# Performance work log

Measured on AMD Instinct MI355X. Metric: run time of the kernel, lower is better.

## Reference

```python
import jax, jax.numpy as jnp
import numpy as np
from jax.ops import segment_sum, segment_max

N, E, FIN, H, C, L, G, ED = 50000, 400000, 256, 4, 64, 3, 25, 2
D = H * C  # 256 = dim*heads


def setup_inputs() -> dict:
    key = jax.random.key(0)
    k = jax.random.split(key, 16)
    s = 0.05
    f = jnp.float32
    return {
        "x": jax.random.normal(k[0], (N, FIN), f),
        "edge_attr": jax.random.uniform(k[1], (E, ED), dtype=f),
        "edge_index": jax.random.randint(k[2], (2, E), 0, N),
        "batch": jnp.sort(jax.random.randint(k[3], (N,), 0, G)),
        "W_pre": jax.random.normal(k[4], (FIN, D), f) * s,
        "b_pre": jnp.zeros((D,), f),
        "W_src": jax.random.normal(k[5], (L, D, D), f) * s,
        "W_dst": jax.random.normal(k[6], (L, D, D), f) * s,
        "W_edge": jax.random.normal(k[7], (L, ED, D), f) * s,
        "att_src": jax.random.normal(k[8], (L, H, C), f) * s,
        "att_dst": jax.random.normal(k[9], (L, H, C), f) * s,
        "att_edge": jax.random.normal(k[10], (L, H, C), f) * s,
        "bias_conv": jnp.zeros((L, D), f),
        "ln_gamma": jnp.ones((L, D), f),
        "ln_beta": jnp.zeros((L, D), f),
        "prelu_a": jnp.full((L, D), 0.25, f),
        "W_post1": jax.random.normal(k[11], (D * (L + 1), D), f) * s,
        "b_post1": jnp.zeros((D,), f),
        "W_post2": jax.random.normal(k[12], (D, D), f) * s,
        "b_post2": jnp.zeros((D,), f),
        "W_risk": jax.random.normal(k[13], (D, 1), f) * s,
        "b_risk": jnp.zeros((1,), f),
    }


def _segment_mean(v, seg, num):
    tot = segment_sum(v, seg, num_segments=num)
    cnt = segment_sum(jnp.ones((v.shape[0], 1), v.dtype), seg, num_segments=num)
    return tot / jnp.maximum(cnt, 1.0)


def _layer_norm(h, g, b, eps=1e-5):
    mu = jnp.mean(h, -1, keepdims=True)
    var = jnp.var(h, -1, keepdims=True)
    return (h - mu) * jax.lax.rsqrt(var + eps) * g + b


def _gat_forward(x, edge_attr, edge_index, batch, params):
    (W_pre, b_pre, W_src, W_dst, W_edge, att_src, att_dst, att_edge,
     bias_conv, ln_gamma, ln_beta, prelu_a,
     W_post1, b_post1, W_post2, b_post2, W_risk, b_risk) = params
    row, col = edge_index[0], edge_index[1]  # src -> dst
    # preprocess: project raw node features to D = dim*heads
    h = x @ W_pre + b_pre  # [N, D]
    concat = [_segment_mean(h, batch, G)]  # x0_glob
    for l in range(L):  # fixed small layer count
        xs = (h @ W_src[l]).reshape(N, H, C)
        xd = (h @ W_dst[l]).reshape(N, H, C)
        ea = (edge_attr @ W_edge[l]).reshape(E, H, C)
        # edge-wise attention logits [E, H]
        a = ((xs * att_src[l]).sum(-1)[row]
             + (xd * att_dst[l]).sum(-1)[col]
             + (ea * att_edge[l]).sum(-1))
        a = jax.nn.leaky_relu(a, 0.2)
        # segment softmax over destination nodes
        m = segment_max(a, col, num_segments=N)
        w = jnp.exp(a - m[col])
        z = segment_sum(w, col, num_segments=N)
        alpha = w / (z[col] + 1e-16)  # [E, H]
        # weighted message passing: gather src feats, scatter-add to dst
        out = segment_sum(xs[row] * alpha[:, :, None], col, num_segments=N)
        out = out.reshape(N, D) + bias_conv[l]
        # per-graph LayerNorm loop == single row-wise LayerNorm
        out = _layer_norm(out, ln_gamma[l], ln_beta[l])
        # channel-wise PReLU
        out = jnp.where(out > 0, out, prelu_a[l] * out)
        concat.append(_segment_mean(out, batch, G))
        h = out + h  # residual_connection == 'Y'
    xc = jnp.concatenate(concat, axis=1)  # [G, D*(L+1)]
    p = jax.nn.relu(xc @ W_post1 + b_post1)
    p = jax.nn.relu(p @ W_post2 + b_post2)
    return p @ W_risk + b_risk  # [G, 1] risk


def reference(x, edge_attr, edge_index, batch, W_pre, b_pre, W_src, W_dst,
              W_edge, att_src, att_dst, att_edge, bias_conv, ln_gamma,
              ln_beta, prelu_a, W_post1, b_post1, W_post2, b_post2,
              W_risk, b_risk):
    params = (W_pre, b_pre, W_src, W_dst, W_edge, att_src, att_dst, att_edge,
              bias_conv, ln_gamma, ln_beta, prelu_a,
              W_post1, b_post1, W_post2, b_post2, W_risk, b_risk)
    return _gat_forward(x, edge_attr, edge_index, batch, params)
```

## Files before the change

kernel.cpp:

```cpp
#include <hip/hip_runtime.h>
#include <math.h>

#define NN 50000
#define NPAD 50048
#define EE 400000
#define DD 256
#define HH 4
#define CC 64
#define LL 3
#define GG 25

typedef _Float16 half4_t __attribute__((ext_vector_type(4)));
typedef _Float16 half8_t __attribute__((ext_vector_type(8)));
typedef float f32x4_t __attribute__((ext_vector_type(4)));

__global__ __launch_bounds__(256) void gemm_mfma(
    const _Float16* __restrict__ Ahi, const _Float16* __restrict__ Alo,
    const _Float16* __restrict__ Bhi, const _Float16* __restrict__ Blo,
    const float* __restrict__ bias, float* __restrict__ C, int N)
{
  __shared__ _Float16 lds[4][128][32];
  const int t = threadIdx.x;
  const int wave = t >> 6, lane = t & 63;
  const int m0 = blockIdx.x * 128, bn0 = blockIdx.y * 128;
  const int wm = wave >> 1, wn = wave & 1;

  f32x4_t acc[4][4];
#pragma unroll
  for (int i = 0; i < 4; i++)
#pragma unroll
    for (int j = 0; j < 4; j++) acc[i][j] = (f32x4_t){0.f, 0.f, 0.f, 0.f};

  const int l15 = lane & 15, kg = lane >> 4;
  int aoff[4], boff[4];
#pragma unroll
  for (int tr = 0; tr < 4; tr++) {
    int r = wm * 64 + tr * 16 + l15;
    aoff[tr] = r * 64 + ((kg ^ ((r >> 1) & 3)) * 16);
    int n = wn * 64 + tr * 16 + l15;
    boff[tr] = n * 64 + ((kg ^ ((n >> 1) & 3)) * 16);
  }

  const _Float16* gsrc[4];
  gsrc[0] = Ahi + (size_t)m0 * 256;
  gsrc[1] = Alo + (size_t)m0 * 256;
  gsrc[2] = Bhi + (size_t)bn0 * 256;
  gsrc[3] = Blo + (size_t)bn0 * 256;

  const char* lbase = (const char*)&lds[0][0][0];

  for (int k0 = 0; k0 < DD; k0 += 32) {
    __syncthreads();
#pragma unroll
    for (int b = 0; b < 4; b++) {
#pragma unroll
      for (int c = 0; c < 2; c++) {
        int rowbase = (wave << 5) + (c << 4);
        const _Float16* g = gsrc[b] + (size_t)(rowbase + (lane >> 2)) * 256
                            + k0 + (lane & 3) * 8;
        char* l = (char*)lbase + b * 8192 + rowbase * 64;
        __builtin_amdgcn_global_load_lds(
            (const __attribute__((address_space(1))) void*)g,
            (__attribute__((address_space(3))) void*)l, 16, 0, 0);
      }
    }
    __syncthreads();

    half8_t ah[4], al[4], bh[4], bl[4];
#pragma unroll
    for (int i = 0; i < 4; i++) {
      ah[i] = *(const half8_t*)(lbase + 0 * 8192 + aoff[i]);
      al[i] = *(const half8_t*)(lbase + 1 * 8192 + aoff[i]);
      bh[i] = *(const half8_t*)(lbase + 2 * 8192 + boff[i]);
      bl[i] = *(const half8_t*)(lbase + 3 * 8192 + boff[i]);
    }
#pragma unroll
    for (int i = 0; i < 4; i++)
#pragma unroll
      for (int j = 0; j < 4; j++) {
        acc[i][j] = __builtin_amdgcn_mfma_f32_16x16x32_f16(ah[i], bh[j], acc[i][j], 0, 0, 0);
        acc[i][j] = __builtin_amdgcn_mfma_f32_16x16x32_f16(ah[i], bl[j], acc[i][j], 0, 0, 0);
        acc[i][j] = __builtin_amdgcn_mfma_f32_16x16x32_f16(al[i], bh[j], acc[i][j], 0, 0, 0);
      }
  }

#pragma unroll
  for (int i = 0; i < 4; i++) {
    int rb = m0 + wm * 64 + i * 16 + (lane >> 4) * 4;
#pragma unroll
    for (int j = 0; j < 4; j++) {
      int col = bn0 + wn * 64 + j * 16 + l15;
      float bv = bias ? bias[col] : 0.f;
#pragma unroll
      for (int q = 0; q < 4; q++) {
        int r = rb + q;
        if (r < N) C[(size_t)r * DD + col] = acc[i][j][q] + bv;
      }
    }
  }
}

__global__ __launch_bounds__(256) void split_f16(
    const float* __restrict__ src, _Float16* __restrict__ hi,
    _Float16* __restrict__ lo, int N)
{
  int f = blockIdx.x * 256 + threadIdx.x;
  if (f >= N * 64) return;
  int m = f >> 6, q = f & 63;
  float4 v = *(const float4*)(src + (size_t)f * 4);
  int gp = (q >> 1) ^ ((m >> 1) & 3);
  int off = m * 256 + gp * 8 + (q & 1) * 4;
  half4_t h4, l4;
  h4[0] = (_Float16)v.x; l4[0] = (_Float16)(v.x - (float)h4[0]);
  h4[1] = (_Float16)v.y; l4[1] = (_Float16)(v.y - (float)h4[1]);
  h4[2] = (_Float16)v.z; l4[2] = (_Float16)(v.z - (float)h4[2]);
  h4[3] = (_Float16)v.w; l4[3] = (_Float16)(v.w - (float)h4[3]);
  *(half4_t*)(hi + off) = h4;
  *(half4_t*)(lo + off) = l4;
}

__global__ void prep_w(const float* __restrict__ W, _Float16* __restrict__ bhi,
                       _Float16* __restrict__ blo)
{
  int n = blockIdx.x, k = threadIdx.x;
  float v = W[(size_t)k * DD + n];
  _Float16 h = (_Float16)v, l = (_Float16)(v - (float)h);
  int kp = (((k >> 3) ^ ((n >> 1) & 3)) << 3) | (k & 7);
  bhi[(size_t)n * DD + kp] = h;
  blo[(size_t)n * DD + kp] = l;
}

__global__ void prep_att(const float* __restrict__ Ws, const float* __restrict__ Wd,
                         const float* __restrict__ We, const float* __restrict__ as_,
                         const float* __restrict__ ad_, const float* __restrict__ ae_,
                         float* __restrict__ wmat, float* __restrict__ wea)
{
  int l = blockIdx.x;
  int t = threadIdx.x;
  for (int idx = t; idx < DD * 8; idx += 256) {
    int k = idx >> 3, hd = idx & 7;
    const float* W; const float* att; int hh;
    if (hd < 4) { W = Ws; att = as_; hh = hd; }
    else        { W = Wd; att = ad_; hh = hd - 4; }
    const float* wrow = W + (size_t)l * DD * DD + (size_t)k * DD + hh * CC;
    const float* arow = att + l * DD + hh * CC;
    float s = 0.f;
#pragma unroll 4
    for (int c = 0; c < CC; c++) s = fmaf(wrow[c], arow[c], s);
    wmat[(size_t)l * DD * 8 + idx] = s;
  }
  if (t < 8) {
    int d = t >> 2, hh = t & 3;
    const float* wrow = We + (size_t)l * 2 * DD + (size_t)d * DD + hh * CC;
    const float* arow = ae_ + l * DD + hh * CC;
    float s = 0.f;
#pragma unroll 4
    for (int c = 0; c < CC; c++) s = fmaf(wrow[c], arow[c], s);
    wea[l * 8 + d * 4 + hh] = s;
  }
}

__global__ void graph_bounds(const int* __restrict__ batch, int* __restrict__ goff,
                             int N, int G)
{
  int g = threadIdx.x;
  if (g > G) return;
  int lo = 0, hi = N;
  while (lo < hi) { int mid = (lo + hi) >> 1; if (batch[mid] < g) lo = mid + 1; else hi = mid; }
  goff[g] = lo;
}

__global__ void hist_col(const int* __restrict__ ei, int* __restrict__ deg, int E)
{
  int e = blockIdx.x * 256 + threadIdx.x;
  if (e < E) atomicAdd(&deg[ei[E + e]], 1);
}

__global__ void scan1(const int* __restrict__ deg, int* __restrict__ incl,
                      int* __restrict__ bsum, int N)
{
  __shared__ int sm[256];
  int b = blockIdx.x, t = threadIdx.x;
  int i = b * 256 + t;
  int v = (i < N) ? deg[i] : 0;
  sm[t] = v;
  __syncthreads();
  for (int off = 1; off < 256; off <<= 1) {
    int add = (t >= off) ? sm[t - off] : 0;
    __syncthreads();
    sm[t] += add;
    __syncthreads();
  }
  if (i < N) incl[i] = sm[t];
  if (t == 255) bsum[b] = sm[255];
}

__global__ void scan2(int* __restrict__ bsum, int nb)
{
  if (threadIdx.x == 0 && blockIdx.x == 0) {
    int run = 0;
    for (int i = 0; i < nb; i++) { int v = bsum[i]; bsum[i] = run; run += v; }
  }
}

__global__ void scan3(const int* __restrict__ deg, const int* __restrict__ incl,
                      const int* __restrict__ bsum, int* __restrict__ rowptr,
                      int* __restrict__ cur, int N, int E)
{
  int i = blockIdx.x * 256 + threadIdx.x;
  if (i < N) {
    int ex = incl[i] - deg[i] + bsum[blockIdx.x];
    rowptr[i] = ex;
    cur[i] = ex;
  }
  if (i == 0) rowptr[N] = E;
}

__global__ void scatter_edges(const int* __restrict__ ei, const float* __restrict__ eattr,
                              int* __restrict__ cur, int* __restrict__ srow,
                              float2* __restrict__ sea, int E)
{
  int e = blockIdx.x * 256 + threadIdx.x;
  if (e < E) {
    int c = ei[E + e];
    int p = atomicAdd(&cur[c], 1);
    srow[p] = ei[e];
    sea[p] = ((const float2*)eattr)[e];
  }
}

__global__ __launch_bounds__(256) void att_proj(
    const float* __restrict__ h, const float* __restrict__ wmatL,
    float* __restrict__ asrc, float* __restrict__ adst, int N)
{
  __shared__ float Hs[32][260];
  __shared__ float Wm[DD * 8];
  int t = threadIdx.x;
  for (int i = t; i < DD * 8; i += 256) Wm[i] = wmatL[i];
  int n0 = blockIdx.x * 32;
  for (int i = t; i < 32 * 64; i += 256) {
    int n = i >> 6, c4 = i & 63;
    float4 v = {0.f, 0.f, 0.f, 0.f};
    if (n0 + n < N) v = *(const float4*)(h + (size_t)(n0 + n) * DD + c4 * 4);
    Hs[n][c4 * 4 + 0] = v.x; Hs[n][c4 * 4 + 1] = v.y;
    Hs[n][c4 * 4 + 2] = v.z; Hs[n][c4 * 4 + 3] = v.w;
  }
  __syncthreads();
  int n = t >> 3, hd = t & 7;
  float s0 = 0, s1 = 0, s2 = 0, s3 = 0;
  for (int k = 0; k < DD; k += 4) {
    s0 = fmaf(Hs[n][k + 0], Wm[(k + 0) * 8 + hd], s0);
    s1 = fmaf(Hs[n][k + 1], Wm[(k + 1) * 8 + hd], s1);
    s2 = fmaf(Hs[n][k + 2], Wm[(k + 2) * 8 + hd], s2);
    s3 = fmaf(Hs[n][k + 3], Wm[(k + 3) * 8 + hd], s3);
  }
  float s = (s0 + s1) + (s2 + s3);
  int gn = n0 + n;
  if (gn < N) {
    if (hd < 4) asrc[gn * 4 + hd] = s;
    else        adst[gn * 4 + (hd - 4)] = s;
  }
}

__global__ __launch_bounds__(256) void dst_fused(
    const float* __restrict__ xs, const float* __restrict__ asrc,
    const float* __restrict__ adst, const int* __restrict__ rowptr,
    const int* __restrict__ srow, const float2* __restrict__ sea,
    const float* __restrict__ weaL, const float* __restrict__ biasL,
    const float* __restrict__ gL, const float* __restrict__ bL,
    const float* __restrict__ pL, float* __restrict__ h,
    _Float16* __restrict__ hhi, _Float16* __restrict__ hlo, int N)
{
  int wid = blockIdx.x * 4 + (threadIdx.x >> 6);
  int lane = threadIdx.x & 63;
  if (wid >= N) return;
  const int head = lane >> 4;
  const int start = rowptr[wid];
  const int end = rowptr[wid + 1];
  const float ad = adst[wid * 4 + head];
  const float w0 = weaL[head];
  const float w1 = weaL[4 + head];
  float ax = 0.f, ay = 0.f, az = 0.f, aw = 0.f;
  float z = 0.f;
  int p = start;
  for (; p + 2 <= end; p += 2) {
    int r0 = srow[p], r1 = srow[p + 1];
    float2 e0 = sea[p], e1 = sea[p + 1];
    float s0 = asrc[r0 * 4 + head], s1 = asrc[r1 * 4 + head];
    float4 x0 = *(const float4*)(xs + (size_t)r0 * DD + lane * 4);
    float4 x1 = *(const float4*)(xs + (size_t)r1 * DD + lane * 4);
    float a0 = s0 + ad + e0.x * w0 + e0.y * w1;
    a0 = a0 > 0.f ? a0 : 0.2f * a0;
    float wt0 = expf(a0);
    float a1 = s1 + ad + e1.x * w0 + e1.y * w1;
    a1 = a1 > 0.f ? a1 : 0.2f * a1;
    float wt1 = expf(a1);
    z += wt0 + wt1;
    ax = fmaf(wt0, x0.x, ax); ay = fmaf(wt0, x0.y, ay);
    az = fmaf(wt0, x0.z, az); aw = fmaf(wt0, x0.w, aw);
    ax = fmaf(wt1, x1.x, ax); ay = fmaf(wt1, x1.y, ay);
    az = fmaf(wt1, x1.z, az); aw = fmaf(wt1, x1.w, aw);
  }
  if (p < end) {
    int r = srow[p];
    float2 ea = sea[p];
    float a = asrc[r * 4 + head] + ad + ea.x * w0 + ea.y * w1;
    a = a > 0.f ? a : 0.2f * a;
    float wt = expf(a);
    z += wt;
    float4 xv = *(const float4*)(xs + (size_t)r * DD + lane * 4);
    ax = fmaf(wt, xv.x, ax); ay = fmaf(wt, xv.y, ay);
    az = fmaf(wt, xv.z, az); aw = fmaf(wt, xv.w, aw);
  }
  float inv = 1.f / (z + 1e-16f);
  float4 bi = *(const float4*)(biasL + lane * 4);
  float o0 = ax * inv + bi.x;
  float o1 = ay * inv + bi.y;
  float o2 = az * inv + bi.z;
  float o3 = aw * inv + bi.w;
  float s = (o0 + o1) + (o2 + o3);
  float q = (o0 * o0 + o1 * o1) + (o2 * o2 + o3 * o3);
#pragma unroll
  for (int off = 32; off; off >>= 1) {
    s += __shfl_xor(s, off, 64);
    q += __shfl_xor(q, off, 64);
  }
  float mu = s * (1.f / 256.f);
  float var = q * (1.f / 256.f) - mu * mu;
  float rs = rsqrtf(var + 1e-5f);
  float4 gg = *(const float4*)(gL + lane * 4);
  float4 bb = *(const float4*)(bL + lane * 4);
  float4 pp = *(const float4*)(pL + lane * 4);
  o0 = (o0 - mu) * rs * gg.x + bb.x;  o0 = o0 > 0.f ? o0 : pp.x * o0;
  o1 = (o1 - mu) * rs * gg.y + bb.y;  o1 = o1 > 0.f ? o1 : pp.y * o1;
  o2 = (o2 - mu) * rs * gg.z + bb.z;  o2 = o2 > 0.f ? o2 : pp.z * o2;
  o3 = (o3 - mu) * rs * gg.w + bb.w;  o3 = o3 > 0.f ? o3 : pp.w * o3;
  float4 hv = *(const float4*)(h + (size_t)wid * DD + lane * 4);
  float4 ov;
  ov.x = o0 + hv.x; ov.y = o1 + hv.y; ov.z = o2 + hv.z; ov.w = o3 + hv.w;
  *(float4*)(h + (size_t)wid * DD + lane * 4) = ov;
  if (hhi) {
    int gp = (lane >> 1) ^ ((wid >> 1) & 3);
    int off2 = wid * DD + gp * 8 + (lane & 1) * 4;
    half4_t h4, l4;
    h4[0] = (_Float16)ov.x; l4[0] = (_Float16)(ov.x - (float)h4[0]);
    h4[1] = (_Float16)ov.y; l4[1] = (_Float16)(ov.y - (float)h4[1]);
    h4[2] = (_Float16)ov.z; l4[2] = (_Float16)(ov.z - (float)h4[2]);
    h4[3] = (_Float16)ov.w; l4[3] = (_Float16)(ov.w - (float)h4[3]);
    *(half4_t*)(hhi + off2) = h4;
    *(half4_t*)(hlo + off2) = l4;
  }
}

__global__ void mean_accum(const float* __restrict__ x, const int* __restrict__ goff,
                           float* __restrict__ msum)
{
  int g = blockIdx.x, sp = blockIdx.y, t = threadIdx.x;
  int lo = goff[g], hi = goff[g + 1];
  int cnt = hi - lo;
  if (cnt <= 0) return;
  int per = (cnt + gridDim.y - 1) / gridDim.y;
  int st = lo + sp * per;
  int en = min(hi, st + per);
  if (st >= en) return;
  float acc = 0.f;
  for (int n = st; n < en; ++n) acc += x[(size_t)n * DD + t];
  atomicAdd(&msum[g * DD + t], acc);
}

__global__ void mean_fin(const float* __restrict__ msum, const int* __restrict__ goff,
                         float* __restrict__ dst)
{
  int g = blockIdx.x, t = threadIdx.x;
  int cnt = goff[g + 1] - goff[g];
  dst[g * DD + t] = msum[g * DD + t] / fmaxf((float)cnt, 1.f);
}

__global__ __launch_bounds__(256) void head_mlp(
    const float* __restrict__ hmean, const float* __restrict__ W1,
    const float* __restrict__ b1, const float* __restrict__ W2,
    const float* __restrict__ b2, const float* __restrict__ Wr,
    const float* __restrict__ br, float* __restrict__ out)
{
  __shared__ float xc[4 * DD];
  __shared__ float p1[DD];
  __shared__ float red[256];
  int g = blockIdx.x, t = threadIdx.x;
  float m0 = hmean[0 * GG * DD + g * DD + t];
  float m1 = hmean[1 * GG * DD + g * DD + t];
  float m2 = hmean[2 * GG * DD + g * DD + t];
  float m3 = hmean[3 * GG * DD + g * DD + t];
  xc[t] = m0;
  xc[DD + t] = m1 - m0;
  xc[2 * DD + t] = m2 - m1;
  xc[3 * DD + t] = m3 - m2;
  __syncthreads();
  float acc = b1[t];
  for (int k = 0; k < 4 * DD; k++) acc = fmaf(xc[k], W1[(size_t)k * DD + t], acc);
  p1[t] = fmaxf(acc, 0.f);
  __syncthreads();
  float acc2 = b2[t];
  for (int k = 0; k < DD; k++) acc2 = fmaf(p1[k], W2[(size_t)k * DD + t], acc2);
  float v = fmaxf(acc2, 0.f) * Wr[t];
  red[t] = v;
  __syncthreads();
  for (int sdown = 128; sdown; sdown >>= 1) {
    if (t < sdown) red[t] += red[t + sdown];
    __syncthreads();
  }
  if (t == 0) out[g] = red[0] + br[0];
}

extern "C" void kernel_launch(void* const* d_in, const int* in_sizes, int n_in,
                              void* d_out, int out_size, void* d_ws, size_t ws_size,
                              hipStream_t stream)
{
  const float* x        = (const float*)d_in[0];
  const float* eattr    = (const float*)d_in[1];
  const int*   eidx     = (const int*)d_in[2];
  const int*   batch    = (const int*)d_in[3];
  const float* W_pre    = (const float*)d_in[4];
  const float* b_pre    = (const float*)d_in[5];
  const float* W_src    = (const float*)d_in[6];
  const float* W_dst    = (const float*)d_in[7];
  const float* W_edge   = (const float*)d_in[8];
  const float* att_src  = (const float*)d_in[9];
  const float* att_dst  = (const float*)d_in[10];
  const float* att_edge = (const float*)d_in[11];
  const float* bias_conv= (const float*)d_in[12];
  const float* ln_g     = (const float*)d_in[13];
  const float* ln_b     = (const float*)d_in[14];
  const float* prelu    = (const float*)d_in[15];
  const float* W1       = (const float*)d_in[16];
  const float* b1       = (const float*)d_in[17];
  const float* W2       = (const float*)d_in[18];
  const float* b2       = (const float*)d_in[19];
  const float* Wr       = (const float*)d_in[20];
  const float* br       = (const float*)d_in[21];
  float* out = (float*)d_out;

  char* w = (char*)d_ws;
  size_t off = 0;
  auto alloc = [&](size_t bytes) -> char* {
    char* p = w + off;
    off += (bytes + 255) & ~(size_t)255;
    return p;
  };
  float*     h     = (float*)alloc((size_t)NN * DD * 4);
  char*      xsreg = alloc((size_t)NPAD * DD * 4);
  float*     xs    = (float*)xsreg;
  _Float16*  x_hi  = (_Float16*)xsreg;
  _Float16*  x_lo  = (_Float16*)(xsreg + (size_t)NPAD * DD * 2);
  _Float16*  h_hi  = (_Float16*)alloc((size_t)NPAD * DD * 2);
  _Float16*  h_lo  = (_Float16*)alloc((size_t)NPAD * DD * 2);
  _Float16*  bt_hi = (_Float16*)alloc((size_t)4 * DD * DD * 2);
  _Float16*  bt_lo = (_Float16*)alloc((size_t)4 * DD * DD * 2);
  float*  asrc  = (float*)alloc((size_t)NN * HH * 4);
  float*  adst  = (float*)alloc((size_t)NN * HH * 4);
  float*  wmat  = (float*)alloc((size_t)LL * DD * 8 * 4);
  float*  wea   = (float*)alloc((size_t)LL * 8 * 4);
  float*  hmean = (float*)alloc((size_t)(LL + 1) * GG * DD * 4);
  float*  msum  = (float*)alloc((size_t)GG * DD * 4);
  float2* sea   = (float2*)alloc((size_t)EE * 8);
  int*    goff  = (int*)alloc((GG + 1) * 4);
  int*    deg   = (int*)alloc((size_t)NN * 4);
  int*    rowptr= (int*)alloc((size_t)(NN + 1) * 4);
  int*    cur   = (int*)alloc((size_t)NN * 4);
  int*    incl  = (int*)alloc((size_t)NN * 4);
  int*    bsum  = (int*)alloc(256 * 4);
  int*    srow  = (int*)alloc((size_t)EE * 4);
  if (off > ws_size) return;

  prep_att<<<dim3(LL), dim3(256), 0, stream>>>(W_src, W_dst, W_edge, att_src,
                                               att_dst, att_edge, wmat, wea);
  prep_w<<<dim3(DD), dim3(DD), 0, stream>>>(W_pre, bt_hi, bt_lo);
  for (int l = 0; l < LL; l++)
    prep_w<<<dim3(DD), dim3(DD), 0, stream>>>(W_src + (size_t)l * DD * DD,
                                              bt_hi + (size_t)(l + 1) * DD * DD,
                                              bt_lo + (size_t)(l + 1) * DD * DD);
  graph_bounds<<<dim3(1), dim3(32), 0, stream>>>(batch, goff, NN, GG);
  hipMemsetAsync(deg, 0, (size_t)NN * 4, stream);
  hist_col<<<dim3((EE + 255) / 256), dim3(256), 0, stream>>>(eidx, deg, EE);
  int nb = (NN + 255) / 256;
  scan1<<<dim3(nb), dim3(256), 0, stream>>>(deg, incl, bsum, NN);
  scan2<<<dim3(1), dim3(1), 0, stream>>>(bsum, nb);
  scan3<<<dim3(nb), dim3(256), 0, stream>>>(deg, incl, bsum, rowptr, cur, NN, EE);
  scatter_edges<<<dim3((EE + 255) / 256), dim3(256), 0, stream>>>(eidx, eattr, cur,
                                                                  srow, sea, EE);

  split_f16<<<dim3((NN * 64 + 255) / 256), dim3(256), 0, stream>>>(x, x_hi, x_lo, NN);
  dim3 gg((NN + 127) / 128, 2);
  gemm_mfma<<<gg, dim3(256), 0, stream>>>(x_hi, x_lo, bt_hi, bt_lo, b_pre, h, NN);
  split_f16<<<dim3((NN * 64 + 255) / 256), dim3(256), 0, stream>>>(h, h_hi, h_lo, NN);
  hipMemsetAsync(msum, 0, (size_t)GG * DD * 4, stream);
  mean_accum<<<dim3(GG, 16), dim3(DD), 0, stream>>>(h, goff, msum);
  mean_fin<<<dim3(GG), dim3(DD), 0, stream>>>(msum, goff, hmean);

  for (int l = 0; l < LL; l++) {
    gemm_mfma<<<gg, dim3(256), 0, stream>>>(h_hi, h_lo,
                                            bt_hi + (size_t)(l + 1) * DD * DD,
                                            bt_lo + (size_t)(l + 1) * DD * DD,
                                            (const float*)nullptr, xs, NN);
    att_proj<<<dim3((NN + 31) / 32), dim3(256), 0, stream>>>(h, wmat + (size_t)l * DD * 8,
                                                             asrc, adst, NN);
    bool ws = (l < LL - 1);
    dst_fused<<<dim3((NN + 3) / 4), dim3(256), 0, stream>>>(
        xs, asrc, adst, rowptr, srow, sea, wea + l * 8, bias_conv + l * DD,
        ln_g + l * DD, ln_b + l * DD, prelu + l * DD, h,
        ws ? h_hi : (_Float16*)nullptr, ws ? h_lo : (_Float16*)nullptr, NN);
    hipMemsetAsync(msum, 0, (size_t)GG * DD * 4, stream);
    mean_accum<<<dim3(GG, 16), dim3(DD), 0, stream>>>(h, goff, msum);
    mean_fin<<<dim3(GG), dim3(DD), 0, stream>>>(msum, goff,
                                                hmean + (size_t)(l + 1) * GG * DD);
  }

  head_mlp<<<dim3(GG), dim3(256), 0, stream>>>(hmean, W1, b1, W2, b2, Wr, br, out);
}
```

Measured before the change: 982.4 us.

## Double-buffer GEMM LDS, unroll edge loop, fuse next-layer attention projection

```diff
diff --git a/kernel.cpp b/kernel.cpp
--- a/kernel.cpp
+++ b/kernel.cpp
@@ -19,7 +19,7 @@
     const _Float16* __restrict__ Bhi, const _Float16* __restrict__ Blo,
     const float* __restrict__ bias, float* __restrict__ C, int N)
 {
-  __shared__ _Float16 lds[4][128][32];
+  __shared__ _Float16 lds[2][4][128][32];
   const int t = threadIdx.x;
   const int wave = t >> 6, lane = t & 63;
   const int m0 = blockIdx.x * 128, bn0 = blockIdx.y * 128;
@@ -47,32 +47,39 @@
   gsrc[2] = Bhi + (size_t)bn0 * 256;
   gsrc[3] = Blo + (size_t)bn0 * 256;
 
-  const char* lbase = (const char*)&lds[0][0][0];
-
-  for (int k0 = 0; k0 < DD; k0 += 32) {
-    __syncthreads();
+  char* lbase = (char*)&lds[0][0][0][0];
+  const int rowbase0 = (wave << 5);
+
+  auto stage = [&](int buf, int k0) {
 #pragma unroll
     for (int b = 0; b < 4; b++) {
 #pragma unroll
       for (int c = 0; c < 2; c++) {
-        int rowbase = (wave << 5) + (c << 4);
+        int rowbase = rowbase0 + (c << 4);
         const _Float16* g = gsrc[b] + (size_t)(rowbase + (lane >> 2)) * 256
                             + k0 + (lane & 3) * 8;
-        char* l = (char*)lbase + b * 8192 + rowbase * 64;
+        char* l = lbase + (size_t)(buf * 4 + b) * 8192 + rowbase * 64;
         __builtin_amdgcn_global_load_lds(
             (const __attribute__((address_space(1))) void*)g,
             (__attribute__((address_space(3))) void*)l, 16, 0, 0);
       }
     }
-    __syncthreads();
-
+  };
+
+  stage(0, 0);
+  __syncthreads();
+  int cur = 0;
+  for (int k0 = 0; k0 < DD; k0 += 32) {
+    if (k0 + 32 < DD) stage(cur ^ 1, k0 + 32);
+
+    const char* lb = lbase + (size_t)cur * 4 * 8192;
     half8_t ah[4], al[4], bh[4], bl[4];
 #pragma unroll
     for (int i = 0; i < 4; i++) {
-      ah[i] = *(const half8_t*)(lbase + 0 * 8192 + aoff[i]);
-      al[i] = *(const half8_t*)(lbase + 1 * 8192 + aoff[i]);
-      bh[i] = *(const half8_t*)(lbase + 2 * 8192 + boff[i]);
-      bl[i] = *(const half8_t*)(lbase + 3 * 8192 + boff[i]);
+      ah[i] = *(const half8_t*)(lb + 0 * 8192 + aoff[i]);
+      al[i] = *(const half8_t*)(lb + 1 * 8192 + aoff[i]);
+      bh[i] = *(const half8_t*)(lb + 2 * 8192 + boff[i]);
+      bl[i] = *(const half8_t*)(lb + 3 * 8192 + boff[i]);
     }
 #pragma unroll
     for (int i = 0; i < 4; i++)
@@ -82,6 +89,8 @@
         acc[i][j] = __builtin_amdgcn_mfma_f32_16x16x32_f16(ah[i], bl[j], acc[i][j], 0, 0, 0);
         acc[i][j] = __builtin_amdgcn_mfma_f32_16x16x32_f16(al[i], bh[j], acc[i][j], 0, 0, 0);
       }
+    __syncthreads();
+    cur ^= 1;
   }
 
 #pragma unroll
@@ -269,7 +278,9 @@
     const float* __restrict__ weaL, const float* __restrict__ biasL,
     const float* __restrict__ gL, const float* __restrict__ bL,
     const float* __restrict__ pL, float* __restrict__ h,
-    _Float16* __restrict__ hhi, _Float16* __restrict__ hlo, int N)
+    _Float16* __restrict__ hhi, _Float16* __restrict__ hlo,
+    const float* __restrict__ wnext, float* __restrict__ asrcN,
+    float* __restrict__ adstN, int N)
 {
   int wid = blockIdx.x * 4 + (threadIdx.x >> 6);
   int lane = threadIdx.x & 63;
@@ -283,30 +294,51 @@
   float ax = 0.f, ay = 0.f, az = 0.f, aw = 0.f;
   float z = 0.f;
   int p = start;
+  for (; p + 4 <= end; p += 4) {
+    int r0 = srow[p], r1 = srow[p + 1], r2 = srow[p + 2], r3 = srow[p + 3];
+    float2 e0 = sea[p], e1 = sea[p + 1], e2 = sea[p + 2], e3 = sea[p + 3];
+    float s0 = asrc[r0 * 4 + head], s1 = asrc[r1 * 4 + head];
+    float s2 = asrc[r2 * 4 + head], s3 = asrc[r3 * 4 + head];
+    float4 x0 = *(const float4*)(xs + (size_t)r0 * DD + lane * 4);
+    float4 x1 = *(const float4*)(xs + (size_t)r1 * DD + lane * 4);
+    float4 x2 = *(const float4*)(xs + (size_t)r2 * DD + lane * 4);
+    float4 x3 = *(const float4*)(xs + (size_t)r3 * DD + lane * 4);
+    float a0 = s0 + ad + e0.x * w0 + e0.y * w1; a0 = a0 > 0.f ? a0 : 0.2f * a0;
+    float a1 = s1 + ad + e1.x * w0 + e1.y * w1; a1 = a1 > 0.f ? a1 : 0.2f * a1;
+    float a2 = s2 + ad + e2.x * w0 + e2.y * w1; a2 = a2 > 0.f ? a2 : 0.2f * a2;
+    float a3 = s3 + ad + e3.x * w0 + e3.y * w1; a3 = a3 > 0.f ? a3 : 0.2f * a3;
+    float t0 = __expf(a0), t1 = __expf(a1), t2 = __expf(a2), t3 = __expf(a3);
+    z += (t0 + t1) + (t2 + t3);
+    ax = fmaf(t0, x0.x, ax); ay = fmaf(t0, x0.y, ay);
+    az = fmaf(t0, x0.z, az); aw = fmaf(t0, x0.w, aw);
+    ax = fmaf(t1, x1.x, ax); ay = fmaf(t1, x1.y, ay);
+    az = fmaf(t1, x1.z, az); aw = fmaf(t1, x1.w, aw);
+    ax = fmaf(t2, x2.x, ax); ay = fmaf(t2, x2.y, ay);
+    az = fmaf(t2, x2.z, az); aw = fmaf(t2, x2.w, aw);
+    ax = fmaf(t3, x3.x, ax); ay = fmaf(t3, x3.y, ay);
+    az = fmaf(t3, x3.z, az); aw = fmaf(t3, x3.w, aw);
+  }
   for (; p + 2 <= end; p += 2) {
     int r0 = srow[p], r1 = srow[p + 1];
     float2 e0 = sea[p], e1 = sea[p + 1];
     float s0 = asrc[r0 * 4 + head], s1 = asrc[r1 * 4 + head];
     float4 x0 = *(const float4*)(xs + (size_t)r0 * DD + lane * 4);
     float4 x1 = *(const float4*)(xs + (size_t)r1 * DD + lane * 4);
-    float a0 = s0 + ad + e0.x * w0 + e0.y * w1;
-    a0 = a0 > 0.f ? a0 : 0.2f * a0;
-    float wt0 = expf(a0);
-    float a1 = s1 + ad + e1.x * w0 + e1.y * w1;
-    a1 = a1 > 0.f ? a1 : 0.2f * a1;
-    float wt1 = expf(a1);
-    z += wt0 + wt1;
-    ax = fmaf(wt0, x0.x, ax); ay = fmaf(wt0, x0.y, ay);
-    az = fmaf(wt0, x0.z, az); aw = fmaf(wt0, x0.w, aw);
-    ax = fmaf(wt1, x1.x, ax); ay = fmaf(wt1, x1.y, ay);
-    az = fmaf(wt1, x1.z, az); aw = fmaf(wt1, x1.w, aw);
+    float a0 = s0 + ad + e0.x * w0 + e0.y * w1; a0 = a0 > 0.f ? a0 : 0.2f * a0;
+    float a1 = s1 + ad + e1.x * w0 + e1.y * w1; a1 = a1 > 0.f ? a1 : 0.2f * a1;
+    float t0 = __expf(a0), t1 = __expf(a1);
+    z += t0 + t1;
+    ax = fmaf(t0, x0.x, ax); ay = fmaf(t0, x0.y, ay);
+    az = fmaf(t0, x0.z, az); aw = fmaf(t0, x0.w, aw);
+    ax = fmaf(t1, x1.x, ax); ay = fmaf(t1, x1.y, ay);
+    az = fmaf(t1, x1.z, az); aw = fmaf(t1, x1.w, aw);
   }
   if (p < end) {
     int r = srow[p];
     float2 ea = sea[p];
     float a = asrc[r * 4 + head] + ad + ea.x * w0 + ea.y * w1;
     a = a > 0.f ? a : 0.2f * a;
-    float wt = expf(a);
+    float wt = __expf(a);
     z += wt;
     float4 xv = *(const float4*)(xs + (size_t)r * DD + lane * 4);
     ax = fmaf(wt, xv.x, ax); ay = fmaf(wt, xv.y, ay);
@@ -349,6 +381,25 @@
     h4[3] = (_Float16)ov.w; l4[3] = (_Float16)(ov.w - (float)h4[3]);
     *(half4_t*)(hhi + off2) = h4;
     *(half4_t*)(hlo + off2) = l4;
+  }
+  if (wnext) {
+    float pr[8];
+#pragma unroll
+    for (int hd = 0; hd < 8; hd++) {
+      const float* wr = wnext + (size_t)(lane * 4) * 8 + hd;
+      pr[hd] = ov.x * wr[0] + ov.y * wr[8] + ov.z * wr[16] + ov.w * wr[24];
+    }
+#pragma unroll
+    for (int off = 32; off; off >>= 1) {
+#pragma unroll
+      for (int hd = 0; hd < 8; hd++) pr[hd] += __shfl_xor(pr[hd], off, 64);
+    }
+    if (lane == 0) {
+      asrcN[wid * 4 + 0] = pr[0]; asrcN[wid * 4 + 1] = pr[1];
+      asrcN[wid * 4 + 2] = pr[2]; asrcN[wid * 4 + 3] = pr[3];
+      adstN[wid * 4 + 0] = pr[4]; adstN[wid * 4 + 1] = pr[5];
+      adstN[wid * 4 + 2] = pr[6]; adstN[wid * 4 + 3] = pr[7];
+    }
   }
 }
 
@@ -455,8 +506,10 @@
   _Float16*  h_lo  = (_Float16*)alloc((size_t)NPAD * DD * 2);
   _Float16*  bt_hi = (_Float16*)alloc((size_t)4 * DD * DD * 2);
   _Float16*  bt_lo = (_Float16*)alloc((size_t)4 * DD * DD * 2);
-  float*  asrc  = (float*)alloc((size_t)NN * HH * 4);
-  float*  adst  = (float*)alloc((size_t)NN * HH * 4);
+  float*  asrcA = (float*)alloc((size_t)NN * HH * 4);
+  float*  adstA = (float*)alloc((size_t)NN * HH * 4);
+  float*  asrcB = (float*)alloc((size_t)NN * HH * 4);
+  float*  adstB = (float*)alloc((size_t)NN * HH * 4);
   float*  wmat  = (float*)alloc((size_t)LL * DD * 8 * 4);
   float*  wea   = (float*)alloc((size_t)LL * 8 * 4);
   float*  hmean = (float*)alloc((size_t)(LL + 1) * GG * DD * 4);
@@ -492,6 +545,7 @@
   dim3 gg((NN + 127) / 128, 2);
   gemm_mfma<<<gg, dim3(256), 0, stream>>>(x_hi, x_lo, bt_hi, bt_lo, b_pre, h, NN);
   split_f16<<<dim3((NN * 64 + 255) / 256), dim3(256), 0, stream>>>(h, h_hi, h_lo, NN);
+  att_proj<<<dim3((NN + 31) / 32), dim3(256), 0, stream>>>(h, wmat, asrcA, adstA, NN);
   hipMemsetAsync(msum, 0, (size_t)GG * DD * 4, stream);
   mean_accum<<<dim3(GG, 16), dim3(DD), 0, stream>>>(h, goff, msum);
   mean_fin<<<dim3(GG), dim3(DD), 0, stream>>>(msum, goff, hmean);
@@ -501,13 +555,17 @@
                                             bt_hi + (size_t)(l + 1) * DD * DD,
                                             bt_lo + (size_t)(l + 1) * DD * DD,
                                             (const float*)nullptr, xs, NN);
-    att_proj<<<dim3((NN + 31) / 32), dim3(256), 0, stream>>>(h, wmat + (size_t)l * DD * 8,
-                                                             asrc, adst, NN);
     bool ws = (l < LL - 1);
+    const float* aS = (l & 1) ? asrcB : asrcA;
+    const float* aD = (l & 1) ? adstB : adstA;
+    float* aSN = (l & 1) ? asrcA : asrcB;
+    float* aDN = (l & 1) ? adstA : adstB;
     dst_fused<<<dim3((NN + 3) / 4), dim3(256), 0, stream>>>(
-        xs, asrc, adst, rowptr, srow, sea, wea + l * 8, bias_conv + l * DD,
+        xs, aS, aD, rowptr, srow, sea, wea + l * 8, bias_conv + l * DD,
         ln_g + l * DD, ln_b + l * DD, prelu + l * DD, h,
-        ws ? h_hi : (_Float16*)nullptr, ws ? h_lo : (_Float16*)nullptr, NN);
+        ws ? h_hi : (_Float16*)nullptr, ws ? h_lo : (_Float16*)nullptr,
+        ws ? (wmat + (size_t)(l + 1) * DD * 8) : (const float*)nullptr,
+        aSN, aDN, NN);
     hipMemsetAsync(msum, 0, (size_t)GG * DD * 4, stream);
     mean_accum<<<dim3(GG, 16), dim3(DD), 0, stream>>>(h, goff, msum);
     mean_fin<<<dim3(GG), dim3(DD), 0, stream>>>(msum, goff,
```

Result: faster. 935.7 us (-4.8%).
